# Kernel tuning notes

Measured on AMD Instinct MI355X. Metric: run time of the kernel, lower is better.

The kernel has to match this reference:

```python
import jax, jax.numpy as jnp
import numpy as np


def setup_inputs() -> dict:
    key = jax.random.key(0)
    kx, kw = jax.random.split(key)
    B, IN, OUT = 8192, 1024, 4096
    x = jax.random.normal(kx, (B, IN), dtype=jnp.float32)
    # torch.rand -> uniform [0,1)
    weight = jax.random.uniform(kw, (IN, OUT), dtype=jnp.float32)
    return {"x": x, "weight": weight}


def reference(x, weight):
    # Faithful to: (x.unsqueeze(-1) - weight).pow(2).sum(-2)
    # i.e. out[b, o] = sum_i (x[b, i] - weight[i, o])**2
    # Computed via the squared-distance expansion to avoid the
    # (B, in, out) broadcast intermediate:
    x_sq = jnp.sum(x * x, axis=-1, keepdims=True)          # (B, 1)
    w_sq = jnp.sum(weight * weight, axis=0)                # (OUT,)
    cross = jnp.matmul(x, weight)                          # (B, OUT)
    return x_sq - 2.0 * cross + w_sq
```

## Files before the change

### kernel.cpp

```cpp
#include <hip/hip_runtime.h>
#include <cstdint>
#include <cstddef>

#define B_DIM   8192
#define IN_DIM  1024
#define OUT_DIM 4096
#define KT2     (IN_DIM / 64)

typedef __attribute__((ext_vector_type(8)))  int   i32x8;
typedef __attribute__((ext_vector_type(4)))  int   i32x4;
typedef __attribute__((ext_vector_type(16))) float f32x16;

__device__ __forceinline__ void async_copy16(const void* gptr, void* ldsptr) {
    __builtin_amdgcn_global_load_lds(
        (__attribute__((address_space(1))) void*)gptr,
        (__attribute__((address_space(3))) void*)ldsptr,
        16, 0, 0);
}

__device__ __forceinline__ int pack4_fp8(float a, float b, float c, float d) {
    int pk = __builtin_amdgcn_cvt_pk_fp8_f32(a, b, 0, false);
    pk = __builtin_amdgcn_cvt_pk_fp8_f32(c, d, pk, true);
    return pk;
}


__global__ __launch_bounds__(256) void quant_kernel(
    const float* __restrict__ x, const float* __restrict__ wgt,
    unsigned char* __restrict__ At, unsigned char* __restrict__ Bt,
    float* __restrict__ xsq2,
    float* __restrict__ wsq2)
{
    __shared__ float tile[256 * 33];
    __shared__ float red[4][32];

    const int t = threadIdx.x;
    const int w = t >> 6;
    const int l = t & 63;
    const int b = blockIdx.x;

    if (b < 512) {
        const int mt = b >> 1, kh = b & 1;
        const int m  = mt * 32 + (l & 31);
        float s = 0.0f;
        #pragma unroll
        for (int p = 0; p < 2; ++p) {
            const int kt2 = kh * 8 + w * 2 + p;
            const float* src = x + (size_t)m * IN_DIM + kt2 * 64 + (l >> 5) * 32;
            i32x4 lo, hi;
            #pragma unroll
            for (int j = 0; j < 4; ++j) {
                float4 v = ((const float4*)src)[j];
                s += v.x*v.x + v.y*v.y + v.z*v.z + v.w*v.w;
                lo[j] = pack4_fp8(v.x, v.y, v.z, v.w);
            }
            #pragma unroll
            for (int j = 0; j < 4; ++j) {
                float4 v = ((const float4*)src)[4 + j];
                s += v.x*v.x + v.y*v.y + v.z*v.z + v.w*v.w;
                hi[j] = pack4_fp8(v.x, v.y, v.z, v.w);
            }
            unsigned char* pan = At + ((size_t)mt * KT2 + kt2) * 2048;
            *(i32x4*)(pan + l * 16)        = lo;
            *(i32x4*)(pan + 1024 + l * 16) = hi;
        }
        s += __shfl_down(s, 32, 64);
        if (l < 32) red[w][l] = s;
        __syncthreads();
        if (t < 32)
            xsq2[kh * B_DIM + mt * 32 + t] =
                red[0][t] + red[1][t] + red[2][t] + red[3][t];
    } else {
        const int idx = b - 512;
        const int nt = idx & 127, q = idx >> 7, n0 = nt * 32;

        const int rbase = t >> 2, cg = (t & 3) * 8;
        #pragma unroll
        for (int rep = 0; rep < 4; ++rep) {
            const int r = rbase + rep * 64;
            const float* src = wgt + (size_t)(q * 256 + r) * OUT_DIM + n0 + cg;
            float4 v0 = ((const float4*)src)[0];
            float4 v1 = ((const float4*)src)[1];
            float* d = &tile[r * 33 + cg];
            d[0] = v0.x; d[1] = v0.y; d[2] = v0.z; d[3] = v0.w;
            d[4] = v1.x; d[5] = v1.y; d[6] = v1.z; d[7] = v1.w;
        }
        __syncthreads();

        const int kt2 = q * 4 + w;
        const int n   = l & 31;
        const int kb  = w * 64 + (l >> 5) * 32;
        float s = 0.0f;
        i32x4 lo, hi;
        #pragma unroll
        for (int j4 = 0; j4 < 4; ++j4) {
            float f0 = tile[(kb + j4 * 4 + 0) * 33 + n];
            float f1 = tile[(kb + j4 * 4 + 1) * 33 + n];
            float f2 = tile[(kb + j4 * 4 + 2) * 33 + n];
            float f3 = tile[(kb + j4 * 4 + 3) * 33 + n];
            s += f0*f0 + f1*f1 + f2*f2 + f3*f3;
            lo[j4] = pack4_fp8(f0, f1, f2, f3);
        }
        #pragma unroll
        for (int j4 = 0; j4 < 4; ++j4) {
            float f0 = tile[(kb + 16 + j4 * 4 + 0) * 33 + n];
            float f1 = tile[(kb + 16 + j4 * 4 + 1) * 33 + n];
            float f2 = tile[(kb + 16 + j4 * 4 + 2) * 33 + n];
            float f3 = tile[(kb + 16 + j4 * 4 + 3) * 33 + n];
            s += f0*f0 + f1*f1 + f2*f2 + f3*f3;
            hi[j4] = pack4_fp8(f0, f1, f2, f3);
        }
        unsigned char* pan = Bt + ((size_t)nt * KT2 + kt2) * 2048;
        *(i32x4*)(pan + l * 16)        = lo;
        *(i32x4*)(pan + 1024 + l * 16) = hi;

        s += __shfl_down(s, 32, 64);
        if (l < 32) red[w][l] = s;
        __syncthreads();
        if (t < 32)
            wsq2[q * OUT_DIM + n0 + t] =
                red[0][t] + red[1][t] + red[2][t] + red[3][t];
    }
}

__global__ __launch_bounds__(256, 2) void rbf_gemm_kernel(
    const unsigned char* __restrict__ At,
    const unsigned char* __restrict__ Bt,
    const float* __restrict__ xsq2,
    const float* __restrict__ wsq2,
    float* __restrict__ out)
{
    __shared__ __align__(16) unsigned char sm[73728];

    const int t    = threadIdx.x;
    const int w    = t >> 6;
    const int l    = t & 63;
    const int l32  = l & 31;
    const int half = l >> 5;

    const int wg  = blockIdx.y * 64 + blockIdx.x;
    const int swz = (wg & 7) * 128 + (wg >> 3);
    const int bm  = swz >> 4;
    const int bn  = swz & 15;

    f32x16 acc[4][2];
    #pragma unroll
    for (int mi = 0; mi < 4; ++mi)
        #pragma unroll
        for (int ni = 0; ni < 2; ++ni)
            #pragma unroll
            for (int r = 0; r < 16; ++r)
                acc[mi][ni][r] = 0.0f;

    const unsigned char* gaBase  = At + (size_t)(bm * 4 + w)      * (KT2 * 2048);
    const unsigned char* gbBase0 = Bt + (size_t)(bn * 8 + w * 2)  * (KT2 * 2048);
    const unsigned char* gbBase1 = gbBase0 + (size_t)(KT2 * 2048);

    auto stage = [&](int buf, int k) {
        unsigned char* As = sm + buf * 24576;
        unsigned char* Bs = As + 8192;
        const unsigned char* ga  = gaBase  + k * 2048;
        const unsigned char* gb0 = gbBase0 + k * 2048;
        const unsigned char* gb1 = gbBase1 + k * 2048;
        #pragma unroll
        for (int h = 0; h < 2; ++h) {
            async_copy16(ga  + h * 1024 + l * 16, As + w * 2048 + h * 1024);
            async_copy16(gb0 + h * 1024 + l * 16, Bs + (w * 2 + 0) * 2048 + h * 1024);
            async_copy16(gb1 + h * 1024 + l * 16, Bs + (w * 2 + 1) * 2048 + h * 1024);
        }
    };

    auto ldfrag = [&](const unsigned char* base, int p) -> i32x8 {
        i32x4 lo = *(const i32x4*)(base + p * 2048 + l * 16);
        i32x4 hi = *(const i32x4*)(base + p * 2048 + 1024 + l * 16);
        i32x8 r;
        r[0] = lo[0]; r[1] = lo[1]; r[2] = lo[2]; r[3] = lo[3];
        r[4] = hi[0]; r[5] = hi[1]; r[6] = hi[2]; r[7] = hi[3];
        return r;
    };

    stage(0, 0);
    stage(1, 1);

    int cb = 0, sb = 2;
    for (int k = 0; k < 16; ++k) {
        if (k < 15) asm volatile("s_waitcnt vmcnt(6)" ::: "memory");
        else        asm volatile("s_waitcnt vmcnt(0)" ::: "memory");
        __builtin_amdgcn_s_barrier();
        __builtin_amdgcn_sched_barrier(0);

        if (k <= 13) stage(sb, k + 2);

        const unsigned char* As = sm + cb * 24576;
        const unsigned char* Bs = As + 8192;
        i32x8 bf0 = ldfrag(Bs, w * 2 + 0);
        i32x8 bf1 = ldfrag(Bs, w * 2 + 1);
        i32x8 af[4];
        #pragma unroll
        for (int mi = 0; mi < 4; ++mi)
            af[mi] = ldfrag(As, mi);

        __builtin_amdgcn_s_setprio(1);
        #pragma unroll
        for (int mi = 0; mi < 4; ++mi) {
            acc[mi][0] = __builtin_amdgcn_mfma_scale_f32_32x32x64_f8f6f4(
                af[mi], bf0, acc[mi][0],
                0, 0,
                0, 0x7F7F7F7F,
                0, 0x7F7F7F7F);
            acc[mi][1] = __builtin_amdgcn_mfma_scale_f32_32x32x64_f8f6f4(
                af[mi], bf1, acc[mi][1],
                0, 0, 0, 0x7F7F7F7F, 0, 0x7F7F7F7F);
        }
        __builtin_amdgcn_s_setprio(0);

        cb = (cb == 2) ? 0 : cb + 1;
        sb = (sb == 2) ? 0 : sb + 1;
    }

    const int ncol = bn * 256 + w * 64 + l32;
    const float wsn0 = wsq2[ncol]      + wsq2[OUT_DIM + ncol]
                     + wsq2[2 * OUT_DIM + ncol]      + wsq2[3 * OUT_DIM + ncol];
    const float wsn1 = wsq2[ncol + 32] + wsq2[OUT_DIM + ncol + 32]
                     + wsq2[2 * OUT_DIM + ncol + 32] + wsq2[3 * OUT_DIM + ncol + 32];
    #pragma unroll
    for (int mi = 0; mi < 4; ++mi) {
        const int mbase = bm * 128 + mi * 32 + 4 * half;
        #pragma unroll
        for (int r2 = 0; r2 < 4; ++r2) {
            #pragma unroll
            for (int r1 = 0; r1 < 4; ++r1) {
                const int m  = mbase + r1 + 8 * r2;
                const float xs = xsq2[m] + xsq2[B_DIM + m];
                float* orow = out + (size_t)m * OUT_DIM + ncol;
                orow[0]  = xs + wsn0 - 2.0f * acc[mi][0][r2 * 4 + r1];
                orow[32] = xs + wsn1 - 2.0f * acc[mi][1][r2 * 4 + r1];
            }
        }
    }
}

extern "C" void kernel_launch(void* const* d_in, const int* in_sizes, int n_in,
                              void* d_out, int out_size, void* d_ws, size_t ws_size,
                              hipStream_t stream)
{
    const float* x   = (const float*)d_in[0];
    const float* wgt = (const float*)d_in[1];
    float* out = (float*)d_out;
    char*  ws  = (char*)d_ws;

    unsigned char* At = (unsigned char*)ws;
    unsigned char* Bt = (unsigned char*)(ws + (size_t)B_DIM * IN_DIM);
    float* xsq2 = (float*)(ws + (size_t)B_DIM * IN_DIM + (size_t)OUT_DIM * IN_DIM);
    float* wsq2 = xsq2 + 2 * B_DIM;

    quant_kernel<<<1024, 256, 0, stream>>>(x, wgt, At, Bt, xsq2, wsq2);
    rbf_gemm_kernel<<<dim3(64, 16), 256, 0, stream>>>(At, Bt, xsq2, wsq2, out);
}
```

Before: 191.5 us.

## Process two N-tiles per workgroup and prefetch next tile during epilogue

The GEMM grid shrinks from 1024 to 512 workgroups, and each workgroup computes two adjacent 128x256 output tiles one after the other. While the first tile's results are written out, the first two k-stages of the second tile are loaded into LDS ahead of time. This hides the epilogue store latency and the pipeline fill behind useful work, and reduces the tail effect from launching more blocks. In exchange there are fewer workgroups to spread across CUs, which may cut parallelism. The waitcnt handling at the seam between the two tiles is also more fragile.

```diff
diff --git a/kernel.cpp b/kernel.cpp
--- a/kernel.cpp
+++ b/kernel.cpp
@@ -138,37 +138,12 @@
     const int l32  = l & 31;
     const int half = l >> 5;
 
-    const int wg  = blockIdx.y * 64 + blockIdx.x;
-    const int swz = (wg & 7) * 128 + (wg >> 3);
-    const int bm  = swz >> 4;
-    const int bn  = swz & 15;
-
-    f32x16 acc[4][2];
-    #pragma unroll
-    for (int mi = 0; mi < 4; ++mi)
-        #pragma unroll
-        for (int ni = 0; ni < 2; ++ni)
-            #pragma unroll
-            for (int r = 0; r < 16; ++r)
-                acc[mi][ni][r] = 0.0f;
-
-    const unsigned char* gaBase  = At + (size_t)(bm * 4 + w)      * (KT2 * 2048);
-    const unsigned char* gbBase0 = Bt + (size_t)(bn * 8 + w * 2)  * (KT2 * 2048);
-    const unsigned char* gbBase1 = gbBase0 + (size_t)(KT2 * 2048);
-
-    auto stage = [&](int buf, int k) {
-        unsigned char* As = sm + buf * 24576;
-        unsigned char* Bs = As + 8192;
-        const unsigned char* ga  = gaBase  + k * 2048;
-        const unsigned char* gb0 = gbBase0 + k * 2048;
-        const unsigned char* gb1 = gbBase1 + k * 2048;
-        #pragma unroll
-        for (int h = 0; h < 2; ++h) {
-            async_copy16(ga  + h * 1024 + l * 16, As + w * 2048 + h * 1024);
-            async_copy16(gb0 + h * 1024 + l * 16, Bs + (w * 2 + 0) * 2048 + h * 1024);
-            async_copy16(gb1 + h * 1024 + l * 16, Bs + (w * 2 + 1) * 2048 + h * 1024);
-        }
-    };
+    const int wg  = blockIdx.x;
+    const int swz = (wg & 7) * 64 + (wg >> 3);
+    const int bm  = swz >> 3;
+    const int bnp = swz & 7;
+
+    const unsigned char* gaBase = At + (size_t)(bm * 4 + w) * (KT2 * 2048);
 
     auto ldfrag = [&](const unsigned char* base, int p) -> i32x8 {
         i32x4 lo = *(const i32x4*)(base + p * 2048 + l * 16);
@@ -179,62 +154,115 @@
         return r;
     };
 
-    stage(0, 0);
-    stage(1, 1);
-
-    int cb = 0, sb = 2;
-    for (int k = 0; k < 16; ++k) {
-        if (k < 15) asm volatile("s_waitcnt vmcnt(6)" ::: "memory");
-        else        asm volatile("s_waitcnt vmcnt(0)" ::: "memory");
-        __builtin_amdgcn_s_barrier();
-        __builtin_amdgcn_sched_barrier(0);
-
-        if (k <= 13) stage(sb, k + 2);
-
-        const unsigned char* As = sm + cb * 24576;
-        const unsigned char* Bs = As + 8192;
-        i32x8 bf0 = ldfrag(Bs, w * 2 + 0);
-        i32x8 bf1 = ldfrag(Bs, w * 2 + 1);
-        i32x8 af[4];
+    #pragma unroll
+    for (int tt = 0; tt < 2; ++tt) {
+        const int bn = bnp * 2 + tt;
+        const unsigned char* gbBase0 = Bt + (size_t)(bn * 8 + w * 2) * (KT2 * 2048);
+        const unsigned char* gbBase1 = gbBase0 + (size_t)(KT2 * 2048);
+
+        auto stage = [&](int buf, int k) {
+            unsigned char* As = sm + buf * 24576;
+            unsigned char* Bs = As + 8192;
+            const unsigned char* ga  = gaBase  + k * 2048;
+            const unsigned char* gb0 = gbBase0 + k * 2048;
+            const unsigned char* gb1 = gbBase1 + k * 2048;
+            #pragma unroll
+            for (int h = 0; h < 2; ++h) {
+                async_copy16(ga  + h * 1024 + l * 16, As + w * 2048 + h * 1024);
+                async_copy16(gb0 + h * 1024 + l * 16, Bs + (w * 2 + 0) * 2048 + h * 1024);
+                async_copy16(gb1 + h * 1024 + l * 16, Bs + (w * 2 + 1) * 2048 + h * 1024);
+            }
+        };
+
+        f32x16 acc[4][2];
         #pragma unroll
         for (int mi = 0; mi < 4; ++mi)
-            af[mi] = ldfrag(As, mi);
-
-        __builtin_amdgcn_s_setprio(1);
+            #pragma unroll
+            for (int ni = 0; ni < 2; ++ni)
+                #pragma unroll
+                for (int r = 0; r < 16; ++r)
+                    acc[mi][ni][r] = 0.0f;
+
+        if (tt == 0) {
+            stage(0, 0);
+            stage(1, 1);
+        }
+
+        int cb = 0, sb = 2;
+        for (int k = 0; k < 16; ++k) {
+            if (tt == 1 && k < 2) {
+            } else if (k < 15) {
+                asm volatile("s_waitcnt vmcnt(6)" ::: "memory");
+            } else {
+                asm volatile("s_waitcnt vmcnt(0)" ::: "memory");
+            }
+            __builtin_amdgcn_s_barrier();
+            __builtin_amdgcn_sched_barrier(0);
+
+            if (k <= 13) stage(sb, k + 2);
+
+            const unsigned char* As = sm + cb * 24576;
+            const unsigned char* Bs = As + 8192;
+            i32x8 bf0 = ldfrag(Bs, w * 2 + 0);
+            i32x8 bf1 = ldfrag(Bs, w * 2 + 1);
+            i32x8 af[4];
+            #pragma unroll
+            for (int mi = 0; mi < 4; ++mi)
+                af[mi] = ldfrag(As, mi);
+
+            __builtin_amdgcn_s_setprio(1);
+            #pragma unroll
+            for (int mi = 0; mi < 4; ++mi) {
+                acc[mi][0] = __builtin_amdgcn_mfma_scale_f32_32x32x64_f8f6f4(
+                    af[mi], bf0, acc[mi][0],
+                    0, 0,
+                    0, 0x7F7F7F7F,
+                    0, 0x7F7F7F7F);
+                acc[mi][1] = __builtin_amdgcn_mfma_scale_f32_32x32x64_f8f6f4(
+                    af[mi], bf1, acc[mi][1],
+                    0, 0, 0, 0x7F7F7F7F, 0, 0x7F7F7F7F);
+            }
+            __builtin_amdgcn_s_setprio(0);
+
+            cb = (cb == 2) ? 0 : cb + 1;
+            sb = (sb == 2) ? 0 : sb + 1;
+        }
+
+        if (tt == 0) {
+            __builtin_amdgcn_s_barrier();
+            const unsigned char* nb0 = Bt + (size_t)((bnp * 2 + 1) * 8 + w * 2) * (KT2 * 2048);
+            const unsigned char* nb1 = nb0 + (size_t)(KT2 * 2048);
+            #pragma unroll
+            for (int k = 0; k < 2; ++k) {
+                unsigned char* As = sm + k * 24576;
+                unsigned char* Bs = As + 8192;
+                #pragma unroll
+                for (int h = 0; h < 2; ++h) {
+                    async_copy16(gaBase + k * 2048 + h * 1024 + l * 16, As + w * 2048 + h * 1024);
+                    async_copy16(nb0    + k * 2048 + h * 1024 + l * 16, Bs + (w * 2 + 0) * 2048 + h * 1024);
+                    async_copy16(nb1    + k * 2048 + h * 1024 + l * 16, Bs + (w * 2 + 1) * 2048 + h * 1024);
+                }
+            }
+        }
+
+        const int ncol = bn * 256 + w * 64 + l32;
+        const float wsn0 = wsq2[ncol]      + wsq2[OUT_DIM + ncol]
+                         + wsq2[2 * OUT_DIM + ncol]      + wsq2[3 * OUT_DIM + ncol];
+        const float wsn1 = wsq2[ncol + 32] + wsq2[OUT_DIM + ncol + 32]
+                         + wsq2[2 * OUT_DIM + ncol + 32] + wsq2[3 * OUT_DIM + ncol + 32];
         #pragma unroll
         for (int mi = 0; mi < 4; ++mi) {
-            acc[mi][0] = __builtin_amdgcn_mfma_scale_f32_32x32x64_f8f6f4(
-                af[mi], bf0, acc[mi][0],
-                0, 0,
-                0, 0x7F7F7F7F,
-                0, 0x7F7F7F7F);
-            acc[mi][1] = __builtin_amdgcn_mfma_scale_f32_32x32x64_f8f6f4(
-                af[mi], bf1, acc[mi][1],
-                0, 0, 0, 0x7F7F7F7F, 0, 0x7F7F7F7F);
-        }
-        __builtin_amdgcn_s_setprio(0);
-
-        cb = (cb == 2) ? 0 : cb + 1;
-        sb = (sb == 2) ? 0 : sb + 1;
-    }
-
-    const int ncol = bn * 256 + w * 64 + l32;
-    const float wsn0 = wsq2[ncol]      + wsq2[OUT_DIM + ncol]
-                     + wsq2[2 * OUT_DIM + ncol]      + wsq2[3 * OUT_DIM + ncol];
-    const float wsn1 = wsq2[ncol + 32] + wsq2[OUT_DIM + ncol + 32]
-                     + wsq2[2 * OUT_DIM + ncol + 32] + wsq2[3 * OUT_DIM + ncol + 32];
-    #pragma unroll
-    for (int mi = 0; mi < 4; ++mi) {
-        const int mbase = bm * 128 + mi * 32 + 4 * half;
-        #pragma unroll
-        for (int r2 = 0; r2 < 4; ++r2) {
-            #pragma unroll
-            for (int r1 = 0; r1 < 4; ++r1) {
-                const int m  = mbase + r1 + 8 * r2;
-                const float xs = xsq2[m] + xsq2[B_DIM + m];
-                float* orow = out + (size_t)m * OUT_DIM + ncol;
-                orow[0]  = xs + wsn0 - 2.0f * acc[mi][0][r2 * 4 + r1];
-                orow[32] = xs + wsn1 - 2.0f * acc[mi][1][r2 * 4 + r1];
+            const int mbase = bm * 128 + mi * 32 + 4 * half;
+            #pragma unroll
+            for (int r2 = 0; r2 < 4; ++r2) {
+                #pragma unroll
+                for (int r1 = 0; r1 < 4; ++r1) {
+                    const int m  = mbase + r1 + 8 * r2;
+                    const float xs = xsq2[m] + xsq2[B_DIM + m];
+                    float* orow = out + (size_t)m * OUT_DIM + ncol;
+                    orow[0]  = xs + wsn0 - 2.0f * acc[mi][0][r2 * 4 + r1];
+                    orow[32] = xs + wsn1 - 2.0f * acc[mi][1][r2 * 4 + r1];
+                }
             }
         }
     }
@@ -255,5 +283,5 @@
     float* wsq2 = xsq2 + 2 * B_DIM;
 
     quant_kernel<<<1024, 256, 0, stream>>>(x, wgt, At, Bt, xsq2, wsq2);
-    rbf_gemm_kernel<<<dim3(64, 16), 256, 0, stream>>>(At, Bt, xsq2, wsq2, out);
-}
+    rbf_gemm_kernel<<<512, 256, 0, stream>>>(At, Bt, xsq2, wsq2, out);
+}
```

Measured after the change: 217.9 us. +13.8%, slower.
